# Kernel optimization log

Measured on AMD Instinct MI355X. Metric: run time of the kernel, lower is better.

## Reference

```python
import jax, jax.numpy as jnp
import numpy as np

L = 4      # n_layers
H = 8      # n_head
DK = 16    # d_k = d_v
DM = 128   # d_model
DI = 512   # d_inner
B = 64
S = 2048
EPS = 1e-6
TEMP = 0.5 * float(np.sqrt(DK))  # ScaledDotProductAttention: 0.5 * d_k**0.5


def _layer_norm(x, g, b):
    mu = jnp.mean(x, axis=-1, keepdims=True)
    var = jnp.mean((x - mu) ** 2, axis=-1, keepdims=True)
    return (x - mu) / jnp.sqrt(var + EPS) * g + b


def _mish(x):
    return x * jnp.tanh(jax.nn.softplus(x))


def _enc_layer(q_in, k_in, v_in, mask, ln1_g, ln1_b, Wq, Wk, Wv, Wfc,
               ln2_g, ln2_b, W1, b1, W2, b2):
    b, l, _ = q_in.shape
    res = q_in
    qn = _layer_norm(q_in, ln1_g, ln1_b)          # only q is layer-normed
    q = (qn   @ Wq).reshape(b, l, H, DK).transpose(0, 2, 1, 3)  # [b,h,l,dk]
    k = (k_in @ Wk).reshape(b, l, H, DK).transpose(0, 2, 1, 3)
    v = (v_in @ Wv).reshape(b, l, H, DK).transpose(0, 2, 1, 3)
    # AvgPool2d((1,2)) pools the last (feature) dim of [b,h,l,dk] by 2
    k = k.reshape(b, H, l, DK // 2, 2).mean(-1)   # [b,h,l,dk/2]
    v = v.reshape(b, H, l, DK // 2, 2).mean(-1)
    # attn = matmul(q.transpose(2,3)/temp, k): contracts over SEQ dim
    attn = jnp.einsum('bhld,bhle->bhde', q, k) / TEMP  # [b,h,dk,dk/2]
    attn = jnp.where(mask[:, None], attn, -1e9)        # mask [b,dk,dk/2]
    attn = jax.nn.softmax(attn, axis=-1)
    out = jnp.einsum('bhde,bhle->bhdl', attn, v)       # [b,h,dk,l]
    # torch: transpose(1,3).view(b,l,-1) -> flatten order (dk, h)
    out = out.transpose(0, 3, 2, 1).reshape(b, l, DK * H)
    out = out @ Wfc + res
    # position-wise FFN with Mish
    res2 = out
    xn = _layer_norm(out, ln2_g, ln2_b)
    h = _mish(xn @ W1 + b1)
    return (h @ W2 + b2) + res2


def setup_inputs() -> dict:
    key = jax.random.key(0)
    ks = jax.random.split(key, 10)
    def nrm(k, shape, scale=0.05):
        return jax.random.normal(k, shape, jnp.float32) * scale
    return {
        'src_seq': jax.random.normal(ks[0], (B, S, 2 * DM), jnp.float32),
        'src_mask': jnp.ones((B, DK, DK // 2), dtype=bool),
        'ln1_g': jnp.ones((L, DM), jnp.float32),
        'ln1_b': jnp.zeros((L, DM), jnp.float32),
        'Wq': nrm(ks[1], (L, DM, H * DK)),
        'Wk': nrm(ks[2], (L, DM, H * DK)),
        'Wv': nrm(ks[3], (L, DM, H * DK)),
        'Wfc': nrm(ks[4], (L, H * DK, DM)),
        'ln2_g': jnp.ones((L, DM), jnp.float32),
        'ln2_b': jnp.zeros((L, DM), jnp.float32),
        'W1': nrm(ks[5], (L, DM, DI)),
        'b1': jnp.zeros((L, DI), jnp.float32),
        'W2': nrm(ks[6], (L, DI, DM)),
        'b2': jnp.zeros((L, DM), jnp.float32),
        'WL2': nrm(ks[7], (2 * DM, DM)),
        'bL2': jnp.zeros((DM,), jnp.float32),
    }


def reference(src_seq, src_mask, ln1_g, ln1_b, Wq, Wk, Wv, Wfc,
              ln2_g, ln2_b, W1, b1, W2, b2, WL2, bL2):
    def lay(i, q, k, v):
        return _enc_layer(q, k, v, src_mask, ln1_g[i], ln1_b[i], Wq[i], Wk[i],
                          Wv[i], Wfc[i], ln2_g[i], ln2_b[i], W1[i], b1[i],
                          W2[i], b2[i])
    m1 = src_seq[:, :, :DM]
    m2 = src_seq[:, :, DM:]
    for i in range(L):
        m1 = lay(i, m1, m1, m1)
    for i in range(L):
        m2 = lay(i, m2, m2, m2)
    # cross stream 1: q from second half, k/v from first half (only layer 0 cross)
    e1 = src_seq[:, :, DM:]
    k1 = src_seq[:, :, :DM]
    for i in range(L):
        e1 = lay(i, e1, k1, k1) if i < 1 else lay(i, e1, e1, e1)
    e2 = src_seq[:, :, :DM]
    k2 = src_seq[:, :, DM:]
    for i in range(L):
        e2 = lay(i, e2, k2, k2) if i < 1 else lay(i, e2, e2, e2)
    enc = jnp.concatenate([e1, e2], axis=2) @ WL2 + bL2
    for i in range(L):
        enc = lay(i, enc, enc, enc)
    return (enc, m1, m2)
```

## Files before the change

kernel.cpp:

```cpp
#include <hip/hip_runtime.h>
#include <math.h>

#define H_    8
#define DK_   16
#define DM_   128
#define DI_   512
#define B_    64
#define S_    2048
#define NTOK  131072
#define EPS_  1e-6f
#define INV_TEMP 0.5f

typedef __attribute__((ext_vector_type(8))) _Float16 half8;
typedef __attribute__((ext_vector_type(4))) _Float16 half4;
typedef __attribute__((ext_vector_type(4))) float f32x4;

struct P4 { const float* p[4]; };

__global__ __launch_bounds__(256) void pack_b(
    const float* __restrict__ W, _Float16* __restrict__ out, int K, int N)
{
    long base = (long)blockIdx.y * K * N;
    int idx = blockIdx.x * 256 + threadIdx.x;
    if (idx >= K * N) return;
    int j = idx & 7;
    int lane = (idx >> 3) & 63;
    int t = idx >> 9;
    int KT = K >> 5;
    int nt = t / KT, kt = t - nt * KT;
    int k = kt * 32 + (lane >> 4) * 8 + j;
    int n = nt * 16 + (lane & 15);
    out[base + idx] = (_Float16)W[base + (long)k * N + n];
}

__global__ __launch_bounds__(256) void pack_fold(
    const float* __restrict__ W, _Float16* __restrict__ out)
{
    long wbase = (long)blockIdx.y * 128 * 128;
    long obase = (long)blockIdx.y * 128 * 64;
    int idx = blockIdx.x * 256 + threadIdx.x;
    int j = idx & 7;
    int lane = (idx >> 3) & 63;
    int t = idx >> 9;
    int nt = t >> 2, kt = t & 3;
    int k = kt * 32 + (lane >> 4) * 8 + j;
    int n = nt * 16 + (lane & 15);
    float v = 0.5f * (W[wbase + (long)k * 128 + 2 * n]
                    + W[wbase + (long)k * 128 + 2 * n + 1]);
    out[obase + idx] = (_Float16)v;
}

__global__ __launch_bounds__(256) void enc_qkv_attn(
    P4 qp, int ldq, P4 kp, int ldk,
    _Float16* __restrict__ v8, float* __restrict__ att,
    const _Float16* __restrict__ Wqp, const _Float16* __restrict__ Wkp,
    const _Float16* __restrict__ Wvp,
    const float* __restrict__ lng, const float* __restrict__ lnb)
{
    __shared__ _Float16 s_xn[64 * 136];
    __shared__ _Float16 s_k[64 * 72];
    __shared__ float s_p[1024];

    const int tid  = threadIdx.x;
    const int w    = tid >> 6;
    const int lane = tid & 63;
    const int quad = lane >> 4, l16 = lane & 15;
    const int bx   = blockIdx.x;
    const int s    = bx >> 11;
    const int blk  = bx & 2047;
    const long tok0 = (long)blk * 64;
    const int b = blk >> 5;
    const int trow = w * 16 + l16;
    const long gtok = tok0 + trow;

    const float* qb = qp.p[s];
    const float* kb = kp.p[s];
    _Float16* v8s = v8 + (long)s * ((long)NTOK * 64) + tok0 * 64;
    float* atts = att + (long)s * (B_ * 1024) + (long)b * 1024;

    for (int i = tid; i < 1024; i += 256) s_p[i] = 0.f;

    half8 xk[4];
    #pragma unroll
    for (int kt = 0; kt < 4; ++kt) {
        f32x4 a = *(const f32x4*)(kb + gtok * (long)ldk + kt * 32 + quad * 8);
        f32x4 c = *(const f32x4*)(kb + gtok * (long)ldk + kt * 32 + quad * 8 + 4);
        #pragma unroll
        for (int r = 0; r < 4; ++r) {
            xk[kt][r]     = (_Float16)a[r];
            xk[kt][r + 4] = (_Float16)c[r];
        }
    }

    #pragma unroll
    for (int nt = 0; nt < 4; ++nt) {
        f32x4 c = {0.f, 0.f, 0.f, 0.f};
        #pragma unroll
        for (int kt = 0; kt < 4; ++kt) {
            half8 wf = *(const half8*)(Wkp + ((nt * 4 + kt) * 64 + lane) * 8);
            c = __builtin_amdgcn_mfma_f32_16x16x32_f16(wf, xk[kt], c, 0, 0, 0);
        }
        half4 hv;
        #pragma unroll
        for (int r = 0; r < 4; ++r) hv[r] = (_Float16)c[r];
        *(half4*)(s_k + trow * 72 + nt * 16 + quad * 4) = hv;
    }

    #pragma unroll
    for (int nt = 0; nt < 4; ++nt) {
        f32x4 c = {0.f, 0.f, 0.f, 0.f};
        #pragma unroll
        for (int kt = 0; kt < 4; ++kt) {
            half8 wf = *(const half8*)(Wvp + ((nt * 4 + kt) * 64 + lane) * 8);
            c = __builtin_amdgcn_mfma_f32_16x16x32_f16(wf, xk[kt], c, 0, 0, 0);
        }
        half4 hv;
        #pragma unroll
        for (int r = 0; r < 4; ++r) hv[r] = (_Float16)c[r];
        *(half4*)(v8s + (long)trow * 64 + nt * 16 + quad * 4) = hv;
    }

    f32x4 xq[8];
    #pragma unroll
    for (int k = 0; k < 8; ++k)
        xq[k] = *(const f32x4*)(qb + gtok * (long)ldq + quad * 32 + k * 4);
    float mu, rs;
    {
        float sm = 0.f;
        #pragma unroll
        for (int k = 0; k < 8; ++k)
            #pragma unroll
            for (int r = 0; r < 4; ++r) sm += xq[k][r];
        sm += __shfl_xor(sm, 16); sm += __shfl_xor(sm, 32);
        mu = sm * (1.f / 128.f);
        float ss = 0.f;
        #pragma unroll
        for (int k = 0; k < 8; ++k)
            #pragma unroll
            for (int r = 0; r < 4; ++r) { float d = xq[k][r] - mu; ss += d * d; }
        ss += __shfl_xor(ss, 16); ss += __shfl_xor(ss, 32);
        rs = rsqrtf(ss * (1.f / 128.f) + EPS_);
    }
    #pragma unroll
    for (int k = 0; k < 8; ++k) {
        f32x4 g  = *(const f32x4*)(lng + quad * 32 + k * 4);
        f32x4 bb = *(const f32x4*)(lnb + quad * 32 + k * 4);
        half4 hv;
        #pragma unroll
        for (int r = 0; r < 4; ++r)
            hv[r] = (_Float16)((xq[k][r] - mu) * rs * g[r] + bb[r]);
        *(half4*)(s_xn + trow * 136 + quad * 32 + k * 4) = hv;
    }

    half8 xn[4];
    #pragma unroll
    for (int kt = 0; kt < 4; ++kt)
        xn[kt] = *(const half8*)(s_xn + trow * 136 + kt * 32 + quad * 8);
    f32x4 qa[8];
    #pragma unroll
    for (int nt = 0; nt < 8; ++nt) {
        f32x4 c = {0.f, 0.f, 0.f, 0.f};
        #pragma unroll
        for (int kt = 0; kt < 4; ++kt) {
            half8 wf = *(const half8*)(Wqp + ((nt * 4 + kt) * 64 + lane) * 8);
            c = __builtin_amdgcn_mfma_f32_16x16x32_f16(wf, xn[kt], c, 0, 0, 0);
        }
        qa[nt] = c;
    }
    #pragma unroll
    for (int nt = 0; nt < 8; ++nt) {
        half4 hv;
        #pragma unroll
        for (int r = 0; r < 4; ++r) hv[r] = (_Float16)qa[nt][r];
        *(half4*)(s_xn + trow * 136 + nt * 16 + quad * 4) = hv;
    }

    __syncthreads();

    {
        const int j = lane;
        const int h0 = j >> 4, h1 = (j + 64) >> 4;
        float p0[8], p1[8];
        #pragma unroll
        for (int e = 0; e < 8; ++e) { p0[e] = 0.f; p1[e] = 0.f; }
        #pragma unroll
        for (int t = 0; t < 16; ++t) {
            int tok = w * 16 + t;
            float q0 = (float)s_xn[tok * 136 + j];
            float q1 = (float)s_xn[tok * 136 + j + 64];
            half8 k0 = *(const half8*)(s_k + tok * 72 + h0 * 8);
            half8 k1 = *(const half8*)(s_k + tok * 72 + h1 * 8);
            #pragma unroll
            for (int e = 0; e < 8; ++e) {
                p0[e] += q0 * (float)k0[e];
                p1[e] += q1 * (float)k1[e];
            }
        }
        #pragma unroll
        for (int ee = 0; ee < 8; ++ee) {
            int e = (ee + (j >> 2)) & 7;
            atomicAdd(&s_p[j * 8 + e], p0[e]);
            atomicAdd(&s_p[(j + 64) * 8 + e], p1[e]);
        }
    }
    __syncthreads();
    for (int i = tid; i < 1024; i += 256)
        atomicAdd(atts + i, s_p[i]);
}

__global__ __launch_bounds__(256) void enc_post_mfma(
    P4 xp, int ldx, P4 op, int ldo,
    const _Float16* __restrict__ v8, const float* __restrict__ att,
    const _Float16* __restrict__ Wfcp,
    const float* __restrict__ lng, const float* __restrict__ lnb,
    const _Float16* __restrict__ W1p, const float* __restrict__ bv1,
    const _Float16* __restrict__ W2p, const float* __restrict__ bv2)
{
    __shared__ float s_att[1024];
    __shared__ _Float16 s_x[128 * 136];

    const int tid  = threadIdx.x;
    const int w    = tid >> 6;
    const int lane = tid & 63;
    const int quad = lane >> 4, l16 = lane & 15;
    const int bx   = blockIdx.x;
    const int s    = bx >> 10;
    const int blk  = bx & 1023;
    const long tok0 = (long)blk * 128;
    const int b = blk >> 4;

    const float* xb = xp.p[s];
    float* ob = (float*)op.p[s];
    const _Float16* v8s = v8 + (long)s * ((long)NTOK * 64) + tok0 * 64;
    const float* atts = att + (long)s * (B_ * 1024) + (long)b * 1024;

    const int trA = w * 16 + l16;
    const int trB = trA + 64;

    if (tid < 128) {
        float sc[8];
        #pragma unroll
        for (int e = 0; e < 8; ++e) sc[e] = atts[tid * 8 + e] * INV_TEMP;
        float m = sc[0];
        #pragma unroll
        for (int e = 1; e < 8; ++e) m = fmaxf(m, sc[e]);
        float sum = 0.f;
        #pragma unroll
        for (int e = 0; e < 8; ++e) { sc[e] = expf(sc[e] - m); sum += sc[e]; }
        float inv = 1.f / sum;
        #pragma unroll
        for (int e = 0; e < 8; ++e) s_att[tid * 8 + e] = sc[e] * inv;
    }
    __syncthreads();

    half8 hvA[8], hvB[8];
    {
        const _Float16* vra = v8s + (long)trA * 64;
        const _Float16* vrb = v8s + (long)trB * 64;
        #pragma unroll
        for (int j = 0; j < 8; ++j) {
            hvA[j] = *(const half8*)(vra + j * 8);
            hvB[j] = *(const half8*)(vrb + j * 8);
        }
    }

    half8 afragA[4], afragB[4];
    {
        float aoA[4][8], aoB[4][8];
        #pragma unroll
        for (int j = 0; j < 8; ++j) {
            #pragma unroll
            for (int kt = 0; kt < 4; ++kt) {
                const float* ar = s_att + (j * 16 + kt * 4 + quad) * 8;
                float4 a0 = *(const float4*)ar;
                float4 a1 = *(const float4*)(ar + 4);
                float vA = (float)hvA[j][0] * a0.x + (float)hvA[j][1] * a0.y
                         + (float)hvA[j][2] * a0.z + (float)hvA[j][3] * a0.w
                         + (float)hvA[j][4] * a1.x + (float)hvA[j][5] * a1.y
                         + (float)hvA[j][6] * a1.z + (float)hvA[j][7] * a1.w;
                float vB = (float)hvB[j][0] * a0.x + (float)hvB[j][1] * a0.y
                         + (float)hvB[j][2] * a0.z + (float)hvB[j][3] * a0.w
                         + (float)hvB[j][4] * a1.x + (float)hvB[j][5] * a1.y
                         + (float)hvB[j][6] * a1.z + (float)hvB[j][7] * a1.w;
                aoA[kt][j] = vA;
                aoB[kt][j] = vB;
            }
        }
        #pragma unroll
        for (int kt = 0; kt < 4; ++kt)
            #pragma unroll
            for (int j = 0; j < 8; ++j) {
                afragA[kt][j] = (_Float16)aoA[kt][j];
                afragB[kt][j] = (_Float16)aoB[kt][j];
            }
    }

    f32x4 yaccA[8], yaccB[8];
    {
        const float* xrowA = xb + (tok0 + trA) * (long)ldx;
        const float* xrowB = xb + (tok0 + trB) * (long)ldx;
        #pragma unroll
        for (int nt = 0; nt < 8; ++nt) {
            yaccA[nt] = *(const f32x4*)(xrowA + nt * 16 + quad * 4);
            yaccB[nt] = *(const f32x4*)(xrowB + nt * 16 + quad * 4);
        }
    }
    #pragma unroll
    for (int nt = 0; nt < 8; ++nt) {
        #pragma unroll
        for (int kt = 0; kt < 4; ++kt) {
            half8 wf = *(const half8*)(Wfcp + ((nt * 4 + kt) * 64 + lane) * 8);
            yaccA[nt] = __builtin_amdgcn_mfma_f32_16x16x32_f16(wf, afragA[kt], yaccA[nt], 0, 0, 0);
            yaccB[nt] = __builtin_amdgcn_mfma_f32_16x16x32_f16(wf, afragB[kt], yaccB[nt], 0, 0, 0);
        }
    }

    float muA, rsA, muB, rsB;
    {
        float smA = 0.f, smB = 0.f;
        #pragma unroll
        for (int nt = 0; nt < 8; ++nt)
            #pragma unroll
            for (int r = 0; r < 4; ++r) { smA += yaccA[nt][r]; smB += yaccB[nt][r]; }
        smA += __shfl_xor(smA, 16); smA += __shfl_xor(smA, 32);
        smB += __shfl_xor(smB, 16); smB += __shfl_xor(smB, 32);
        muA = smA * (1.f / 128.f); muB = smB * (1.f / 128.f);
        float ssA = 0.f, ssB = 0.f;
        #pragma unroll
        for (int nt = 0; nt < 8; ++nt)
            #pragma unroll
            for (int r = 0; r < 4; ++r) {
                float dA = yaccA[nt][r] - muA; ssA += dA * dA;
                float dB = yaccB[nt][r] - muB; ssB += dB * dB;
            }
        ssA += __shfl_xor(ssA, 16); ssA += __shfl_xor(ssA, 32);
        ssB += __shfl_xor(ssB, 16); ssB += __shfl_xor(ssB, 32);
        rsA = rsqrtf(ssA * (1.f / 128.f) + EPS_);
        rsB = rsqrtf(ssB * (1.f / 128.f) + EPS_);
    }

    #pragma unroll
    for (int nt = 0; nt < 8; ++nt) {
        f32x4 g  = *(const f32x4*)(lng + nt * 16 + quad * 4);
        f32x4 bb = *(const f32x4*)(lnb + nt * 16 + quad * 4);
        f32x4 b2v = *(const f32x4*)(bv2 + nt * 16 + quad * 4);
        half4 ha, hb;
        #pragma unroll
        for (int r = 0; r < 4; ++r) {
            ha[r] = (_Float16)((yaccA[nt][r] - muA) * rsA * g[r] + bb[r]);
            hb[r] = (_Float16)((yaccB[nt][r] - muB) * rsB * g[r] + bb[r]);
        }
        *(half4*)(s_x + trA * 136 + nt * 16 + quad * 4) = ha;
        *(half4*)(s_x + trB * 136 + nt * 16 + quad * 4) = hb;
        yaccA[nt] += b2v;
        yaccB[nt] += b2v;
    }
    half8 xfragA[4], xfragB[4];
    #pragma unroll
    for (int kt = 0; kt < 4; ++kt) {
        xfragA[kt] = *(const half8*)(s_x + trA * 136 + kt * 32 + quad * 8);
        xfragB[kt] = *(const half8*)(s_x + trB * 136 + kt * 32 + quad * 8);
    }

    for (int ch = 0; ch < 4; ++ch) {
        #pragma unroll
        for (int tl = 0; tl < 8; ++tl) {
            f32x4 bv = *(const f32x4*)(bv1 + ch * 128 + tl * 16 + quad * 4);
            f32x4 c1A = bv, c1B = bv;
            #pragma unroll
            for (int kt = 0; kt < 4; ++kt) {
                half8 wf = *(const half8*)(W1p + (((ch * 8 + tl) * 4 + kt) * 64 + lane) * 8);
                c1A = __builtin_amdgcn_mfma_f32_16x16x32_f16(wf, xfragA[kt], c1A, 0, 0, 0);
                c1B = __builtin_amdgcn_mfma_f32_16x16x32_f16(wf, xfragB[kt], c1B, 0, 0, 0);
            }
            half4 ha, hb;
            #pragma unroll
            for (int r = 0; r < 4; ++r) {
                float hxA = c1A[r];
                float eA = __expf(fminf(hxA, 30.f));
                float tA = 1.f + eA, t2A = tA * tA;
                ha[r] = (_Float16)(hxA * (t2A - 1.f) * __builtin_amdgcn_rcpf(t2A + 1.f));
                float hxB = c1B[r];
                float eB = __expf(fminf(hxB, 30.f));
                float tB = 1.f + eB, t2B = tB * tB;
                hb[r] = (_Float16)(hxB * (t2B - 1.f) * __builtin_amdgcn_rcpf(t2B + 1.f));
            }
            *(half4*)(s_x + trA * 136 + tl * 16 + quad * 4) = ha;
            *(half4*)(s_x + trB * 136 + tl * 16 + quad * 4) = hb;
        }
        half8 hfragA[4], hfragB[4];
        #pragma unroll
        for (int ks = 0; ks < 4; ++ks) {
            hfragA[ks] = *(const half8*)(s_x + trA * 136 + ks * 32 + quad * 8);
            hfragB[ks] = *(const half8*)(s_x + trB * 136 + ks * 32 + quad * 8);
        }
        #pragma unroll
        for (int nt = 0; nt < 8; ++nt) {
            #pragma unroll
            for (int ks = 0; ks < 4; ++ks) {
                half8 wf = *(const half8*)(W2p + ((nt * 16 + ch * 4 + ks) * 64 + lane) * 8);
                yaccA[nt] = __builtin_amdgcn_mfma_f32_16x16x32_f16(wf, hfragA[ks], yaccA[nt], 0, 0, 0);
                yaccB[nt] = __builtin_amdgcn_mfma_f32_16x16x32_f16(wf, hfragB[ks], yaccB[nt], 0, 0, 0);
            }
        }
    }

    {
        float* orowA = ob + (tok0 + trA) * (long)ldo;
        float* orowB = ob + (tok0 + trB) * (long)ldo;
        #pragma unroll
        for (int nt = 0; nt < 8; ++nt) {
            *(f32x4*)(orowA + nt * 16 + quad * 4) = yaccA[nt];
            *(f32x4*)(orowB + nt * 16 + quad * 4) = yaccB[nt];
        }
    }
}

__global__ __launch_bounds__(256) void enc_combine(
    const float* __restrict__ e1, const float* __restrict__ e2,
    float* __restrict__ outp,
    const float* __restrict__ W, const float* __restrict__ bias)
{
    __shared__ float sc[32 * 256];
    const int tid = threadIdx.x;
    const long tok0 = (long)blockIdx.x * 32;
    #pragma unroll
    for (int r = 0; r < 4; ++r) {
        int u = tid + r * 256;
        int tok = u >> 5, c4 = u & 31;
        *(float4*)(sc + tok * 256 + c4 * 4)       = *(const float4*)(e1 + (tok0 + tok) * 128 + c4 * 4);
        *(float4*)(sc + tok * 256 + 128 + c4 * 4) = *(const float4*)(e2 + (tok0 + tok) * 128 + c4 * 4);
    }
    __syncthreads();
    const int j = tid & 63, tg = tid >> 6;
    float a0[8], a1[8];
    #pragma unroll
    for (int t = 0; t < 8; ++t) { a0[t] = 0.f; a1[t] = 0.f; }
    for (int i = 0; i < 256; i += 4) {
        float w0[4], w1[4];
        #pragma unroll
        for (int u = 0; u < 4; ++u) {
            w0[u] = W[(long)(i + u) * 128 + j];
            w1[u] = W[(long)(i + u) * 128 + j + 64];
        }
        #pragma unroll
        for (int t = 0; t < 8; ++t) {
            float4 xv = *(const float4*)(sc + (tg * 8 + t) * 256 + i);
            a0[t] += xv.x * w0[0] + xv.y * w0[1] + xv.z * w0[2] + xv.w * w0[3];
            a1[t] += xv.x * w1[0] + xv.y * w1[1] + xv.z * w1[2] + xv.w * w1[3];
        }
    }
    float b0 = bias[j], b1 = bias[j + 64];
    #pragma unroll
    for (int t = 0; t < 8; ++t) {
        int tok = tg * 8 + t;
        outp[(tok0 + tok) * 128 + j]      = a0[t] + b0;
        outp[(tok0 + tok) * 128 + j + 64] = a1[t] + b1;
    }
}

extern "C" void kernel_launch(void* const* d_in, const int* in_sizes, int n_in,
                              void* d_out, int out_size, void* d_ws, size_t ws_size,
                              hipStream_t stream)
{
    const float* src  = (const float*)d_in[0];
    const float* ln1g = (const float*)d_in[2];
    const float* ln1b = (const float*)d_in[3];
    const float* Wq   = (const float*)d_in[4];
    const float* Wk   = (const float*)d_in[5];
    const float* Wv   = (const float*)d_in[6];
    const float* Wfc  = (const float*)d_in[7];
    const float* ln2g = (const float*)d_in[8];
    const float* ln2b = (const float*)d_in[9];
    const float* W1   = (const float*)d_in[10];
    const float* b1   = (const float*)d_in[11];
    const float* W2   = (const float*)d_in[12];
    const float* b2   = (const float*)d_in[13];
    const float* WL2  = (const float*)d_in[14];
    const float* bL2  = (const float*)d_in[15];
    float* out = (float*)d_out;

    const long TOKS = (long)NTOK * 128;
    float* ws  = (float*)d_ws;
    float* XE1 = ws;
    float* XE2 = ws + TOKS;
    _Float16* V8 = (_Float16*)(ws + 2 * TOKS);
    float* ATT = (float*)(V8 + 4L * NTOK * 64);
    _Float16* WPfc = (_Float16*)(ATT + 4 * B_ * 1024);
    _Float16* WP1  = WPfc + 4L * 16384;
    _Float16* WP2  = WP1 + 4L * 65536;
    _Float16* WPq  = WP2 + 4L * 65536;
    _Float16* WPk  = WPq + 4L * 16384;
    _Float16* WPv  = WPk + 4L * 8192;
    if (ws_size < 205000000ULL) return;

    float* m1b  = out + TOKS;
    float* m2b  = out + 2 * TOKS;
    float* encb = out;
    const float* bufs[4] = { m1b, m2b, XE1, XE2 };

    pack_b<<<dim3(64, 4),  dim3(256), 0, stream>>>(Wfc, WPfc, 128, 128);
    pack_b<<<dim3(256, 4), dim3(256), 0, stream>>>(W1,  WP1,  128, 512);
    pack_b<<<dim3(256, 4), dim3(256), 0, stream>>>(W2,  WP2,  512, 128);
    pack_b<<<dim3(64, 4),  dim3(256), 0, stream>>>(Wq,  WPq,  128, 128);
    pack_fold<<<dim3(32, 4), dim3(256), 0, stream>>>(Wk, WPk);
    pack_fold<<<dim3(32, 4), dim3(256), 0, stream>>>(Wv, WPv);

    for (int l = 0; l < 4; ++l) {
        hipMemsetAsync(ATT, 0, 4 * B_ * 1024 * sizeof(float), stream);
        P4 qp, kp, op;
        int ldq, ldk;
        if (l == 0) {
            qp = P4{{ src, src + 128, src + 128, src }};  ldq = 256;
            kp = P4{{ src, src + 128, src, src + 128 }};  ldk = 256;
        } else {
            qp = P4{{ bufs[0], bufs[1], bufs[2], bufs[3] }}; ldq = 128;
            kp = qp; ldk = 128;
        }
        op = P4{{ bufs[0], bufs[1], bufs[2], bufs[3] }};
        enc_qkv_attn<<<dim3(4 * 2048), dim3(256), 0, stream>>>(
            qp, ldq, kp, ldk, V8, ATT,
            WPq + (long)l * 16384, WPk + (long)l * 8192, WPv + (long)l * 8192,
            ln1g + l * 128, ln1b + l * 128);
        enc_post_mfma<<<dim3(4 * 1024), dim3(256), 0, stream>>>(
            qp, ldq, op, 128, V8, ATT,
            WPfc + (long)l * 16384, ln2g + l * 128, ln2b + l * 128,
            WP1 + (long)l * 65536, b1 + l * 512,
            WP2 + (long)l * 65536, b2 + l * 128);
    }

    enc_combine<<<dim3(4096), dim3(256), 0, stream>>>(XE1, XE2, encb, WL2, bL2);

    for (int l = 0; l < 4; ++l) {
        hipMemsetAsync(ATT, 0, B_ * 1024 * sizeof(float), stream);
        P4 p = P4{{ encb, encb, encb, encb }};
        enc_qkv_attn<<<dim3(2048), dim3(256), 0, stream>>>(
            p, 128, p, 128, V8, ATT,
            WPq + (long)l * 16384, WPk + (long)l * 8192, WPv + (long)l * 8192,
            ln1g + l * 128, ln1b + l * 128);
        enc_post_mfma<<<dim3(1024), dim3(256), 0, stream>>>(
            p, 128, p, 128, V8, ATT,
            WPfc + (long)l * 16384, ln2g + l * 128, ln2b + l * 128,
            WP1 + (long)l * 65536, b1 + l * 512,
            WP2 + (long)l * 65536, b2 + l * 128);
    }
}
```

Measured before the change: 5.893 ms.

## Widen post-attention tile to 256 tokens, swizzle LDS, stash residual in output

The post-attention kernel now runs 512-thread blocks, each covering 256 tokens, with half the grid. Shared memory becomes one 64KB buffer using an XOR-swizzled layout instead of padded rows, which is meant to avoid bank conflicts. The FFN residual (attention output plus b2) is written to the output buffer right away. The second FFN matmul accumulates into fresh registers and is added to the re-read residual at the end, which should lower the number of live accumulator registers. The cost is an extra global read and write per output element, and a 64KB LDS footprint per block that caps how many blocks fit on a CU.

```diff
diff --git a/kernel.cpp b/kernel.cpp
--- a/kernel.cpp
+++ b/kernel.cpp
@@ -16,6 +16,8 @@
 typedef __attribute__((ext_vector_type(4))) float f32x4;
 
 struct P4 { const float* p[4]; };
+
+#define SWZ(row, bytecol) (((row) << 8) + ((bytecol) ^ (((row) & 7) << 4)))
 
 __global__ __launch_bounds__(256) void pack_b(
     const float* __restrict__ W, _Float16* __restrict__ out, int K, int N)
@@ -208,7 +210,7 @@
         atomicAdd(atts + i, s_p[i]);
 }
 
-__global__ __launch_bounds__(256) void enc_post_mfma(
+__global__ __launch_bounds__(512, 4) void enc_post_mfma(
     P4 xp, int ldx, P4 op, int ldo,
     const _Float16* __restrict__ v8, const float* __restrict__ att,
     const _Float16* __restrict__ Wfcp,
@@ -216,18 +218,19 @@
     const _Float16* __restrict__ W1p, const float* __restrict__ bv1,
     const _Float16* __restrict__ W2p, const float* __restrict__ bv2)
 {
-    __shared__ float s_att[1024];
-    __shared__ _Float16 s_x[128 * 136];
+    __shared__ __align__(16) unsigned char s_raw[65536];
+    float* s_att = (float*)s_raw;
+    char*  s8    = (char*)s_raw;
 
     const int tid  = threadIdx.x;
     const int w    = tid >> 6;
     const int lane = tid & 63;
     const int quad = lane >> 4, l16 = lane & 15;
     const int bx   = blockIdx.x;
-    const int s    = bx >> 10;
-    const int blk  = bx & 1023;
-    const long tok0 = (long)blk * 128;
-    const int b = blk >> 4;
+    const int s    = bx >> 9;
+    const int blk  = bx & 511;
+    const long tok0 = (long)blk * 256;
+    const int b = blk >> 3;
 
     const float* xb = xp.p[s];
     float* ob = (float*)op.p[s];
@@ -235,7 +238,7 @@
     const float* atts = att + (long)s * (B_ * 1024) + (long)b * 1024;
 
     const int trA = w * 16 + l16;
-    const int trB = trA + 64;
+    const int trB = trA + 128;
 
     if (tid < 128) {
         float sc[8];
@@ -339,29 +342,41 @@
         rsB = rsqrtf(ssB * (1.f / 128.f) + EPS_);
     }
 
+    __syncthreads();
+
+    {
+        float* orowA = ob + (tok0 + trA) * (long)ldo;
+        float* orowB = ob + (tok0 + trB) * (long)ldo;
+        #pragma unroll
+        for (int nt = 0; nt < 8; ++nt) {
+            f32x4 g  = *(const f32x4*)(lng + nt * 16 + quad * 4);
+            f32x4 bb = *(const f32x4*)(lnb + nt * 16 + quad * 4);
+            f32x4 b2v = *(const f32x4*)(bv2 + nt * 16 + quad * 4);
+            half4 ha, hb;
+            #pragma unroll
+            for (int r = 0; r < 4; ++r) {
+                ha[r] = (_Float16)((yaccA[nt][r] - muA) * rsA * g[r] + bb[r]);
+                hb[r] = (_Float16)((yaccB[nt][r] - muB) * rsB * g[r] + bb[r]);
+            }
+            *(half4*)(s8 + SWZ(trA, nt * 32 + quad * 8)) = ha;
+            *(half4*)(s8 + SWZ(trB, nt * 32 + quad * 8)) = hb;
+            *(f32x4*)(orowA + nt * 16 + quad * 4) = yaccA[nt] + b2v;
+            *(f32x4*)(orowB + nt * 16 + quad * 4) = yaccB[nt] + b2v;
+        }
+    }
+    half8 xfragA[4], xfragB[4];
+    #pragma unroll
+    for (int kt = 0; kt < 4; ++kt) {
+        xfragA[kt] = *(const half8*)(s8 + SWZ(trA, kt * 64 + quad * 16));
+        xfragB[kt] = *(const half8*)(s8 + SWZ(trB, kt * 64 + quad * 16));
+    }
+
+    f32x4 zaccA[8], zaccB[8];
     #pragma unroll
     for (int nt = 0; nt < 8; ++nt) {
-        f32x4 g  = *(const f32x4*)(lng + nt * 16 + quad * 4);
-        f32x4 bb = *(const f32x4*)(lnb + nt * 16 + quad * 4);
-        f32x4 b2v = *(const f32x4*)(bv2 + nt * 16 + quad * 4);
-        half4 ha, hb;
-        #pragma unroll
-        for (int r = 0; r < 4; ++r) {
-            ha[r] = (_Float16)((yaccA[nt][r] - muA) * rsA * g[r] + bb[r]);
-            hb[r] = (_Float16)((yaccB[nt][r] - muB) * rsB * g[r] + bb[r]);
-        }
-        *(half4*)(s_x + trA * 136 + nt * 16 + quad * 4) = ha;
-        *(half4*)(s_x + trB * 136 + nt * 16 + quad * 4) = hb;
-        yaccA[nt] += b2v;
-        yaccB[nt] += b2v;
-    }
-    half8 xfragA[4], xfragB[4];
-    #pragma unroll
-    for (int kt = 0; kt < 4; ++kt) {
-        xfragA[kt] = *(const half8*)(s_x + trA * 136 + kt * 32 + quad * 8);
-        xfragB[kt] = *(const half8*)(s_x + trB * 136 + kt * 32 + quad * 8);
-    }
-
+        zaccA[nt] = f32x4{0.f, 0.f, 0.f, 0.f};
+        zaccB[nt] = f32x4{0.f, 0.f, 0.f, 0.f};
+    }
     for (int ch = 0; ch < 4; ++ch) {
         #pragma unroll
         for (int tl = 0; tl < 8; ++tl) {
@@ -385,22 +400,22 @@
                 float tB = 1.f + eB, t2B = tB * tB;
                 hb[r] = (_Float16)(hxB * (t2B - 1.f) * __builtin_amdgcn_rcpf(t2B + 1.f));
             }
-            *(half4*)(s_x + trA * 136 + tl * 16 + quad * 4) = ha;
-            *(half4*)(s_x + trB * 136 + tl * 16 + quad * 4) = hb;
+            *(half4*)(s8 + SWZ(trA, tl * 32 + quad * 8)) = ha;
+            *(half4*)(s8 + SWZ(trB, tl * 32 + quad * 8)) = hb;
         }
         half8 hfragA[4], hfragB[4];
         #pragma unroll
         for (int ks = 0; ks < 4; ++ks) {
-            hfragA[ks] = *(const half8*)(s_x + trA * 136 + ks * 32 + quad * 8);
-            hfragB[ks] = *(const half8*)(s_x + trB * 136 + ks * 32 + quad * 8);
+            hfragA[ks] = *(const half8*)(s8 + SWZ(trA, ks * 64 + quad * 16));
+            hfragB[ks] = *(const half8*)(s8 + SWZ(trB, ks * 64 + quad * 16));
         }
         #pragma unroll
         for (int nt = 0; nt < 8; ++nt) {
             #pragma unroll
             for (int ks = 0; ks < 4; ++ks) {
                 half8 wf = *(const half8*)(W2p + ((nt * 16 + ch * 4 + ks) * 64 + lane) * 8);
-                yaccA[nt] = __builtin_amdgcn_mfma_f32_16x16x32_f16(wf, hfragA[ks], yaccA[nt], 0, 0, 0);
-                yaccB[nt] = __builtin_amdgcn_mfma_f32_16x16x32_f16(wf, hfragB[ks], yaccB[nt], 0, 0, 0);
+                zaccA[nt] = __builtin_amdgcn_mfma_f32_16x16x32_f16(wf, hfragA[ks], zaccA[nt], 0, 0, 0);
+                zaccB[nt] = __builtin_amdgcn_mfma_f32_16x16x32_f16(wf, hfragB[ks], zaccB[nt], 0, 0, 0);
             }
         }
     }
@@ -410,8 +425,10 @@
         float* orowB = ob + (tok0 + trB) * (long)ldo;
         #pragma unroll
         for (int nt = 0; nt < 8; ++nt) {
-            *(f32x4*)(orowA + nt * 16 + quad * 4) = yaccA[nt];
-            *(f32x4*)(orowB + nt * 16 + quad * 4) = yaccB[nt];
+            f32x4 ybA = *(const f32x4*)(orowA + nt * 16 + quad * 4);
+            f32x4 ybB = *(const f32x4*)(orowB + nt * 16 + quad * 4);
+            *(f32x4*)(orowA + nt * 16 + quad * 4) = ybA + zaccA[nt];
+            *(f32x4*)(orowB + nt * 16 + quad * 4) = ybB + zaccB[nt];
         }
     }
 }
@@ -522,7 +539,7 @@
             qp, ldq, kp, ldk, V8, ATT,
             WPq + (long)l * 16384, WPk + (long)l * 8192, WPv + (long)l * 8192,
             ln1g + l * 128, ln1b + l * 128);
-        enc_post_mfma<<<dim3(4 * 1024), dim3(256), 0, stream>>>(
+        enc_post_mfma<<<dim3(4 * 512), dim3(512), 0, stream>>>(
             qp, ldq, op, 128, V8, ATT,
             WPfc + (long)l * 16384, ln2g + l * 128, ln2b + l * 128,
             WP1 + (long)l * 65536, b1 + l * 512,
@@ -538,7 +555,7 @@
             p, 128, p, 128, V8, ATT,
             WPq + (long)l * 16384, WPk + (long)l * 8192, WPv + (long)l * 8192,
             ln1g + l * 128, ln1b + l * 128);
-        enc_post_mfma<<<dim3(1024), dim3(256), 0, stream>>>(
+        enc_post_mfma<<<dim3(512), dim3(512), 0, stream>>>(
             p, 128, p, 128, V8, ATT,
             WPfc + (long)l * 16384, ln2g + l * 128, ln2b + l * 128,
             WP1 + (long)l * 65536, b1 + l * 512,
```

Measured after the change: 5.716 ms. -3.0%, faster.
